# Kernel optimization log

Measured on AMD Instinct MI355X. Metric: run time of the kernel, lower is better.

Reference implementation:

```python
import jax, jax.numpy as jnp
import numpy as np
import math

N = 20000      # nodes
E = 320000     # edges
D = 256        # in_dim == out_dim (residual requires equality)
H = 8          # heads
K = D // H     # k_dim = 32
T = 3          # node types
R = 5          # edge (relation) types
C = 16         # output classes
SQRT_K = math.sqrt(K)


def setup_inputs() -> dict:
    key = jax.random.key(0)
    ks = jax.random.split(key, 18)
    x = jax.random.normal(ks[0], (N, D), jnp.float32)
    edge_index = jax.random.randint(ks[1], (2, E), 0, N, jnp.int32)
    node_type = jax.random.randint(ks[2], (N,), 0, T, jnp.int32)
    edge_type = jax.random.randint(ks[3], (E,), 0, R, jnp.int32)
    g_lin = math.sqrt(2.0 / (D + D))
    g_rel = math.sqrt(2.0 / (K + K))
    g_out = math.sqrt(2.0 / (D + C))
    Wk = jax.random.normal(ks[4], (T, D, D), jnp.float32) * g_lin
    bk = jnp.zeros((T, D), jnp.float32)
    Wq = jax.random.normal(ks[5], (T, D, D), jnp.float32) * g_lin
    bq = jnp.zeros((T, D), jnp.float32)
    Wv = jax.random.normal(ks[6], (T, D, D), jnp.float32) * g_lin
    bv = jnp.zeros((T, D), jnp.float32)
    Wa = jax.random.normal(ks[7], (T, D, D), jnp.float32) * g_lin
    ba = jnp.zeros((T, D), jnp.float32)
    rel_prior = jnp.ones((R, H), jnp.float32)
    rel_att = jax.random.normal(ks[8], (R, H, K, K), jnp.float32) * g_rel
    rel_msg = jax.random.normal(ks[9], (R, H, K, K), jnp.float32) * g_rel
    W_out = jax.random.normal(ks[10], (D, C), jnp.float32) * g_out
    b_out = jnp.zeros((C,), jnp.float32)
    return {"x": x, "edge_index": edge_index, "node_type": node_type,
            "edge_type": edge_type, "Wk": Wk, "bk": bk, "Wq": Wq, "bq": bq,
            "Wv": Wv, "bv": bv, "Wa": Wa, "ba": ba, "rel_prior": rel_prior,
            "rel_att": rel_att, "rel_msg": rel_msg, "W_out": W_out, "b_out": b_out}


def _typed_linear(h, W, b, node_type):
    # per-node-type Linear: small fixed loop over T types, masked select
    out = jnp.zeros((h.shape[0], W.shape[2]), h.dtype)
    for t in range(T):
        m = (node_type == t)[:, None]
        out = out + jnp.where(m, h @ W[t] + b[t], 0.0)
    return out


def _hgt_forward(x, edge_index, node_type, edge_type, Wk, bk, Wq, bq, Wv, bv,
                 Wa, ba, rel_prior, rel_att, rel_msg, W_out, b_out):
    src, dst = edge_index[0], edge_index[1]
    # typed projections -> [N, H, K]
    Kn = _typed_linear(x, Wk, bk, node_type).reshape(N, H, K)
    Qn = _typed_linear(x, Wq, bq, node_type).reshape(N, H, K)
    Vn = _typed_linear(x, Wv, bv, node_type).reshape(N, H, K)
    Ke, Qe, Ve = Kn[src], Qn[dst], Vn[src]  # [E, H, K] gathers
    # relation-specific bilinear transforms of K and V (fixed loop over R)
    Kt = jnp.zeros_like(Ke)
    Mt = jnp.zeros_like(Ve)
    for r in range(R):
        m = (edge_type == r)[:, None, None]
        Kt = Kt + jnp.where(m, jnp.einsum('ehk,hkl->ehl', Ke, rel_att[r]), 0.0)
        Mt = Mt + jnp.where(m, jnp.einsum('ehk,hkl->ehl', Ve, rel_msg[r]), 0.0)
    # attention logits with relation prior, scaled by sqrt(k_dim)
    logits = (Qe * Kt).sum(-1) * rel_prior[edge_type] / SQRT_K  # [E, H]
    # segment softmax over incoming edges per destination node
    mx = jax.ops.segment_max(logits, dst, num_segments=N)       # [N, H]
    ex = jnp.exp(logits - mx[dst])
    sm = jax.ops.segment_sum(ex, dst, num_segments=N)           # [N, H]
    att = ex / sm[dst]                                          # [E, H]
    # weighted messages, scatter-add aggregation
    msg = (Mt * att[:, :, None]).reshape(E, D)
    aggr = jax.ops.segment_sum(msg, dst, num_segments=N)        # [N, D]
    # update: ELU, typed output linear, residual
    h = jax.nn.elu(aggr)
    h = _typed_linear(h, Wa, ba, node_type) + x
    # final classifier + log_softmax
    return jax.nn.log_softmax(h @ W_out + b_out, axis=1)


def reference(x, edge_index, node_type, edge_type, Wk, bk, Wq, bq, Wv, bv,
              Wa, ba, rel_prior, rel_att, rel_msg, W_out, b_out):
    return _hgt_forward(x, edge_index, node_type, edge_type, Wk, bk, Wq, bq,
                        Wv, bv, Wa, ba, rel_prior, rel_att, rel_msg, W_out, b_out)
```

## Files before the change

### kernel.cpp

```cpp
#include <hip/hip_runtime.h>
#include <hip/hip_bf16.h>
#include <math.h>

#define NN 20000
#define NE 320000
#define DD 256
#define NH 8
#define KK 32
#define NR 5
#define NC 16
#define NB2 391

typedef unsigned short u16;
typedef unsigned int u32;
typedef __attribute__((ext_vector_type(8))) short bf16x8;
typedef __attribute__((ext_vector_type(4))) float f32x4;

__device__ __forceinline__ float bf2f(u16 v){ return __uint_as_float(((u32)v)<<16); }
__device__ __forceinline__ u16 f2bf(float f){
  u32 u = __float_as_uint(f);
  return (u16)((u + 0x7FFFu + ((u>>16)&1u)) >> 16);
}

__global__ void k_pre1(const int* __restrict__ ntype, const int* __restrict__ ei,
                       const int* __restrict__ etype, int* __restrict__ cnt,
                       int* __restrict__ off2, int* __restrict__ perm){
  int b = blockIdx.x;
  if(b < 79){
    int n = b*256 + threadIdx.x;
    int t = (n < NN) ? ntype[n] : -1;
    int lane = threadIdx.x & 63;
    #pragma unroll
    for(int tt=0; tt<3; tt++){
      unsigned long long mask = __ballot(t == tt);
      int leader = __ffsll((long long)mask) - 1;
      if(lane == leader) atomicAdd(&cnt[tt], __popcll(mask));
    }
  } else if(b < 1329){
    int e = (b-79)*256 + threadIdx.x;
    if(e < NE) atomicAdd(&off2[ei[NE + e]*NR + etype[e]], 1);
  } else {
    int i = (b-1329)*256 + threadIdx.x;
    if(i < 20096) perm[i] = -1;
  }
}

__global__ __launch_bounds__(256) void k_pre2(int* __restrict__ off2, int* __restrict__ bsum,
                                              const int* __restrict__ cnt, int* __restrict__ boff){
  if(blockIdx.x == NB2){
    if(threadIdx.x == 0){
      int a = (cnt[0]+31)&~31;
      int bb = (cnt[1]+31)&~31;
      boff[0]=0; boff[1]=a; boff[2]=a+bb;
    }
    return;
  }
  __shared__ int sh[256];
  int t = threadIdx.x;
  int i = blockIdx.x*256 + t;
  int v = (i < NN*NR) ? off2[i] : 0;
  sh[t] = v;
  __syncthreads();
  for(int off=1; off<256; off<<=1){
    int val = (t >= off) ? sh[t-off] : 0;
    __syncthreads();
    sh[t] += val;
    __syncthreads();
  }
  if(i < NN*NR) off2[i] = sh[t] - v;
  if(t == 255) bsum[blockIdx.x] = sh[255];
}
__global__ __launch_bounds__(512) void k_scan2(int* __restrict__ bsum, int* __restrict__ off2){
  __shared__ int sh[512];
  int t = threadIdx.x;
  int v = (t < NB2) ? bsum[t] : 0;
  sh[t] = v;
  __syncthreads();
  for(int off=1; off<512; off<<=1){
    int val = (t >= off) ? sh[t-off] : 0;
    __syncthreads();
    sh[t] += val;
    __syncthreads();
  }
  if(t < NB2) bsum[t] = sh[t] - v;
  if(t == 511) off2[NN*NR] = sh[511];
}
__global__ void k_pre3(int* __restrict__ off2, const int* __restrict__ bsum,
                       const int* __restrict__ ntype, const int* __restrict__ boff,
                       int* __restrict__ bcur, int* __restrict__ perm,
                       int* __restrict__ pos2){
  int b = blockIdx.x;
  if(b < NB2){
    int i = b*256 + threadIdx.x;
    if(i < NN*NR) off2[i] += bsum[b];
  } else {
    int n = (b-NB2)*256 + threadIdx.x;
    int t = (n < NN) ? ntype[n] : -1;
    int lane = threadIdx.x & 63;
    #pragma unroll
    for(int tt=0; tt<3; tt++){
      unsigned long long mask = __ballot(t == tt);
      if(t == tt){
        int rank = __popcll(mask & ((1ull<<lane)-1ull));
        int leader = __ffsll((long long)mask) - 1;
        int base = 0;
        if(lane == leader) base = atomicAdd(&bcur[tt], __popcll(mask));
        base = __shfl(base, leader);
        int p = boff[tt] + base + rank;
        perm[p] = n;
        pos2[n] = p;
      }
    }
  }
}

__global__ __launch_bounds__(256) void k_work1(
    const int* __restrict__ ei, const int* __restrict__ etype,
    int* __restrict__ off2, int* __restrict__ packed,
    const float* __restrict__ x, u16* __restrict__ xb,
    const float* __restrict__ Wk, const float* __restrict__ Wq,
    const float* __restrict__ Wv, const float* __restrict__ Wa,
    u16* __restrict__ Wtk, u16* __restrict__ Wtq,
    u16* __restrict__ Wtv, u16* __restrict__ Wta,
    const float* __restrict__ rmsg, const float* __restrict__ ratt,
    const float* __restrict__ prior, const float* __restrict__ Wo,
    u16* __restrict__ Mtm, u16* __restrict__ Atb, u16* __restrict__ Wot)
{
  __shared__ float tile[32][33];
  int b = blockIdx.x;
  if(b < 1250){
    int e = b*256 + threadIdx.x;
    if(e < NE){
      int pos = atomicAdd(&off2[ei[NE+e]*NR + etype[e]], 1);
      packed[pos] = ei[e];
    }
  } else if(b < 3750){
    int i = (b-1250)*256 + threadIdx.x;
    float4 v0 = ((const float4*)x)[i*2+0];
    float4 v1 = ((const float4*)x)[i*2+1];
    uint4 o;
    o.x = (u32)f2bf(v0.x) | ((u32)f2bf(v0.y)<<16);
    o.y = (u32)f2bf(v0.z) | ((u32)f2bf(v0.w)<<16);
    o.z = (u32)f2bf(v1.x) | ((u32)f2bf(v1.y)<<16);
    o.w = (u32)f2bf(v1.z) | ((u32)f2bf(v1.w)<<16);
    ((uint4*)xb)[i] = o;
  } else if(b < 4518){
    int bp = b - 3750;
    int bx = bp & 7, by = (bp>>3) & 7, z = bp >> 6;
    int tensor = z/3, t = z%3;
    const float* W = (tensor==0) ? Wk : (tensor==1) ? Wq : (tensor==2) ? Wv : Wa;
    u16* O = (tensor==0) ? Wtk : (tensor==1) ? Wtq : (tensor==2) ? Wtv : Wta;
    int i0 = bx*32, j0 = by*32;
    int rr = threadIdx.x>>5, cc = threadIdx.x&31;
    #pragma unroll
    for(int p=0;p<4;p++)
      tile[rr+p*8][cc] = W[t*65536 + (i0+rr+p*8)*256 + j0+cc];
    __syncthreads();
    #pragma unroll
    for(int p=0;p<4;p++)
      O[t*65536 + (j0+rr+p*8)*256 + i0+cc] = f2bf(tile[cc][rr+p*8]);
  } else {
    int bp = b - 4518;
    if(bp < 160){
      int idx = bp*256 + threadIdx.x;
      int l = idx & 31, k = (idx >> 5) & 31, rh = idx >> 10;
      Mtm[(rh*32 + l)*32 + k] = f2bf(rmsg[idx]);
    } else if(bp < 320){
      int idx = (bp-160)*256 + threadIdx.x;
      int rh = idx >> 10;
      float scale = prior[rh] * 0.17677669529663687f;
      Atb[idx] = f2bf(ratt[idx] * scale);
    } else {
      int idx = (bp-320)*256 + threadIdx.x;
      int c = idx & 15, k = idx >> 4;
      Wot[c*DD + k] = f2bf(Wo[k*NC + c]);
    }
  }
}

#define XSP 264
__global__ __launch_bounds__(256) void k_projqa(
    const u16* __restrict__ xb, const int* __restrict__ perm, const int* __restrict__ boff,
    const u16* __restrict__ Wtk, const u16* __restrict__ Wtq, const u16* __restrict__ Wtv,
    const float* __restrict__ bk, const float* __restrict__ bq, const float* __restrict__ bv,
    const u16* __restrict__ Atb,
    u16* __restrict__ KVn, u16* __restrict__ QA)
{
  __shared__ u16 smem[32*XSP];
  __shared__ int gids[32];
  int tid = threadIdx.x;
  int ts = (blockIdx.x >> 1)*32;
  int cb = (blockIdx.x & 1)*128;
  int t = (ts >= boff[2]) ? 2 : (ts >= boff[1]) ? 1 : 0;
  if(tid < 32) gids[tid] = perm[ts + tid];
  __syncthreads();
  #pragma unroll
  for(int it=0; it<4; it++){
    int q = tid + it*256;
    int row = q >> 5, c = q & 31;
    int g = gids[row];
    uint4 v = make_uint4(0,0,0,0);
    if(g >= 0) v = ((const uint4*)(xb + (size_t)g*DD))[c];
    ((uint4*)(smem + row*XSP))[c] = v;
  }
  __syncthreads();
  int lane = tid & 63;
  int w = tid >> 6;
  int quad = lane >> 4;
  int l16 = lane & 15;
  f32x4 accK[2][2], accQ[2][2], accV[2][2];
  #pragma unroll
  for(int mt=0;mt<2;mt++)
    #pragma unroll
    for(int nt=0;nt<2;nt++){
      accK[mt][nt]=(f32x4)(0.f); accQ[mt][nt]=(f32x4)(0.f); accV[mt][nt]=(f32x4)(0.f);
    }
  const u16* wkp = Wtk + (size_t)t*65536;
  const u16* wqp = Wtq + (size_t)t*65536;
  const u16* wvp = Wtv + (size_t)t*65536;
  #pragma unroll
  for(int kk=0; kk<8; kk++){
    int kb = kk*32 + quad*8;
    bf16x8 a0 = *(const bf16x8*)(smem + l16*XSP + kb);
    bf16x8 a1 = *(const bf16x8*)(smem + (16+l16)*XSP + kb);
    #pragma unroll
    for(int nt=0; nt<2; nt++){
      int n = cb + w*32 + nt*16 + l16;
      bf16x8 bK = *(const bf16x8*)(wkp + (size_t)n*DD + kb);
      bf16x8 bQ = *(const bf16x8*)(wqp + (size_t)n*DD + kb);
      bf16x8 bV = *(const bf16x8*)(wvp + (size_t)n*DD + kb);
      accK[0][nt] = __builtin_amdgcn_mfma_f32_16x16x32_bf16(a0, bK, accK[0][nt], 0,0,0);
      accK[1][nt] = __builtin_amdgcn_mfma_f32_16x16x32_bf16(a1, bK, accK[1][nt], 0,0,0);
      accQ[0][nt] = __builtin_amdgcn_mfma_f32_16x16x32_bf16(a0, bQ, accQ[0][nt], 0,0,0);
      accQ[1][nt] = __builtin_amdgcn_mfma_f32_16x16x32_bf16(a1, bQ, accQ[1][nt], 0,0,0);
      accV[0][nt] = __builtin_amdgcn_mfma_f32_16x16x32_bf16(a0, bV, accV[0][nt], 0,0,0);
      accV[1][nt] = __builtin_amdgcn_mfma_f32_16x16x32_bf16(a1, bV, accV[1][nt], 0,0,0);
    }
  }
  __syncthreads();
  #pragma unroll
  for(int nt=0; nt<2; nt++){
    int lc = w*32 + nt*16 + l16;
    int colg = cb + lc;
    int kvo = ((lc >> 2)*8 + (lc & 3));
    float bkv = bk[t*DD+colg], bvv = bv[t*DD+colg];
    #pragma unroll
    for(int mt=0; mt<2; mt++){
      #pragma unroll
      for(int reg=0; reg<4; reg++){
        int row = mt*16 + quad*4 + reg;
        smem[row*XSP + kvo]     = f2bf(accK[mt][nt][reg] + bkv);
        smem[row*XSP + kvo + 4] = f2bf(accV[mt][nt][reg] + bvv);
      }
    }
  }
  __syncthreads();
  #pragma unroll
  for(int it=0; it<4; it++){
    int q = tid + it*256;
    int row = q >> 5, c = q & 31;
    int g = gids[row];
    if(g >= 0)
      *(uint4*)(KVn + (size_t)g*512 + (cb>>2)*8 + c*8) = ((uint4*)(smem + row*XSP))[c];
  }
  __syncthreads();
  #pragma unroll
  for(int nt=0; nt<2; nt++){
    int lc = w*32 + nt*16 + l16;
    float bqv = bq[t*DD + cb + lc];
    #pragma unroll
    for(int mt=0; mt<2; mt++){
      #pragma unroll
      for(int reg=0; reg<4; reg++){
        int row = mt*16 + quad*4 + reg;
        smem[row*XSP + lc] = f2bf(accQ[mt][nt][reg] + bqv);
      }
    }
  }
  __syncthreads();
  int h = (cb >> 5) + w;
  bf16x8 qf0 = *(const bf16x8*)(smem + l16*XSP + w*32 + quad*8);
  bf16x8 qf1 = *(const bf16x8*)(smem + (16+l16)*XSP + w*32 + quad*8);
  for(int r=0; r<NR; r++){
    f32x4 acc[2][2];
    #pragma unroll
    for(int mt=0;mt<2;mt++)
      #pragma unroll
      for(int nt=0;nt<2;nt++) acc[mt][nt]=(f32x4)(0.f);
    const u16* ap = Atb + (size_t)(r*NH + h)*1024;
    bf16x8 b0 = *(const bf16x8*)(ap + l16*32 + quad*8);
    bf16x8 b1 = *(const bf16x8*)(ap + (16+l16)*32 + quad*8);
    acc[0][0] = __builtin_amdgcn_mfma_f32_16x16x32_bf16(qf0, b0, acc[0][0], 0,0,0);
    acc[0][1] = __builtin_amdgcn_mfma_f32_16x16x32_bf16(qf0, b1, acc[0][1], 0,0,0);
    acc[1][0] = __builtin_amdgcn_mfma_f32_16x16x32_bf16(qf1, b0, acc[1][0], 0,0,0);
    acc[1][1] = __builtin_amdgcn_mfma_f32_16x16x32_bf16(qf1, b1, acc[1][1], 0,0,0);
    __syncthreads();
    #pragma unroll
    for(int mt=0; mt<2; mt++)
      #pragma unroll
      for(int nt=0; nt<2; nt++)
        #pragma unroll
        for(int reg=0; reg<4; reg++){
          int row = mt*16 + quad*4 + reg;
          smem[row*XSP + w*32 + nt*16 + l16] = f2bf(acc[mt][nt][reg]);
        }
    __syncthreads();
    #pragma unroll
    for(int it=0; it<2; it++){
      int q = tid + it*256;
      int row = q >> 4, c = q & 15;
      int g = gids[row];
      if(g >= 0)
        *(uint4*)(QA + ((size_t)g*NR + r)*DD + cb + c*8) = ((uint4*)(smem + row*XSP))[c];
    }
  }
}

#define VSP 264
__global__ __launch_bounds__(256) void k_edge(
    const u16* __restrict__ KVn, const u16* __restrict__ QA,
    const int* __restrict__ off2, const int* __restrict__ packed,
    const int* __restrict__ pos2, u16* __restrict__ aggrV)
{
  int lane = threadIdx.x & 63;
  int n = blockIdx.x*4 + (threadIdx.x >> 6);
  if(n >= NN) return;
  int off = lane*4;
  float4 qa[NR];
  {
    const u16* qp = QA + (size_t)n*NR*DD + off;
    #pragma unroll
    for(int r=0;r<NR;r++){
      ushort4 q = *(const ushort4*)(qp + r*DD);
      qa[r] = make_float4(bf2f(q.x),bf2f(q.y),bf2f(q.z),bf2f(q.w));
    }
  }
  int eb[NR+1];
  eb[0] = (n==0) ? 0 : off2[n*NR - 1];
  #pragma unroll
  for(int i=1;i<=NR;i++) eb[i] = off2[n*NR + i - 1];
  float4 acc[NR];
  float s = 0.f;
  int lo8 = lane*8;

  #define EDGE_DOT(kv, q, dd) \
    { float k0=__uint_as_float((kv).x<<16), k1=__uint_as_float((kv).x&0xffff0000u); \
      float k2=__uint_as_float((kv).y<<16), k3=__uint_as_float((kv).y&0xffff0000u); \
      dd = k0*(q).x + k1*(q).y + k2*(q).z + k3*(q).w; }
  #define EDGE_ACC(kv, p, a) \
    { float v0=__uint_as_float((kv).z<<16), v1=__uint_as_float((kv).z&0xffff0000u); \
      float v2=__uint_as_float((kv).w<<16), v3=__uint_as_float((kv).w&0xffff0000u); \
      (a).x += (p)*v0; (a).y += (p)*v1; (a).z += (p)*v2; (a).w += (p)*v3; }
  #define RED3(d) { d += __shfl_xor(d,1); d += __shfl_xor(d,2); d += __shfl_xor(d,4); }

  #pragma unroll
  for(int r=0;r<NR;r++){
    float4 q = qa[r];
    float4 a = make_float4(0.f,0.f,0.f,0.f);
    int e = eb[r], end = eb[r+1];
    for(; e+4 <= end; e += 4){
      int s0 = packed[e], s1 = packed[e+1], s2 = packed[e+2], s3 = packed[e+3];
      uint4 kv0 = *(const uint4*)(KVn + (size_t)s0*512 + lo8);
      uint4 kv1 = *(const uint4*)(KVn + (size_t)s1*512 + lo8);
      uint4 kv2 = *(const uint4*)(KVn + (size_t)s2*512 + lo8);
      uint4 kv3 = *(const uint4*)(KVn + (size_t)s3*512 + lo8);
      float d0,d1,d2,d3;
      EDGE_DOT(kv0,q,d0); EDGE_DOT(kv1,q,d1); EDGE_DOT(kv2,q,d2); EDGE_DOT(kv3,q,d3);
      RED3(d0); RED3(d1); RED3(d2); RED3(d3);
      float p0=__expf(d0), p1=__expf(d1), p2=__expf(d2), p3=__expf(d3);
      s += p0 + p1 + p2 + p3;
      EDGE_ACC(kv0,p0,a); EDGE_ACC(kv1,p1,a); EDGE_ACC(kv2,p2,a); EDGE_ACC(kv3,p3,a);
    }
    if(e+2 <= end){
      int s0 = packed[e], s1 = packed[e+1];
      uint4 kv0 = *(const uint4*)(KVn + (size_t)s0*512 + lo8);
      uint4 kv1 = *(const uint4*)(KVn + (size_t)s1*512 + lo8);
      float d0,d1;
      EDGE_DOT(kv0,q,d0); EDGE_DOT(kv1,q,d1);
      RED3(d0); RED3(d1);
      float p0=__expf(d0), p1=__expf(d1);
      s += p0 + p1;
      EDGE_ACC(kv0,p0,a); EDGE_ACC(kv1,p1,a);
      e += 2;
    }
    if(e < end){
      int s0 = packed[e];
      uint4 kv0 = *(const uint4*)(KVn + (size_t)s0*512 + lo8);
      float d0;
      EDGE_DOT(kv0,q,d0);
      RED3(d0);
      float p0=__expf(d0);
      s += p0;
      EDGE_ACC(kv0,p0,a);
    }
    acc[r] = a;
  }
  #undef EDGE_DOT
  #undef EDGE_ACC
  #undef RED3
  float inv = (s > 0.f) ? (1.f/s) : 0.f;
  int p = pos2[n];
  u16* op = aggrV + (size_t)p*NR*DD + off;
  #pragma unroll
  for(int r=0;r<NR;r++){
    ushort4 o;
    o.x=f2bf(acc[r].x*inv); o.y=f2bf(acc[r].y*inv);
    o.z=f2bf(acc[r].z*inv); o.w=f2bf(acc[r].w*inv);
    *(ushort4*)(op + r*DD) = o;
  }
}

__global__ __launch_bounds__(256) void k_mo(
    const u16* __restrict__ aggrV, const u16* __restrict__ Mtm,
    const float* __restrict__ x,
    const int* __restrict__ perm, const int* __restrict__ boff,
    const u16* __restrict__ Wta, const float* __restrict__ ba,
    const u16* __restrict__ Wot, const float* __restrict__ bo,
    float* __restrict__ out)
{
  __shared__ u16 Vs[32*VSP];
  __shared__ u16 hs[32*VSP];
  __shared__ u16 h2s[32*VSP];
  __shared__ int gids[32];
  int tid = threadIdx.x;
  int ts = blockIdx.x*32;
  int t = (ts >= boff[2]) ? 2 : (ts >= boff[1]) ? 1 : 0;
  if(tid < 32) gids[tid] = perm[ts + tid];
  __syncthreads();
  int lane = tid & 63, w = tid >> 6, quad = lane >> 4, l16 = lane & 15;

  f32x4 macc[2][2][2];
  #pragma unroll
  for(int hh=0;hh<2;hh++)
    #pragma unroll
    for(int mt=0;mt<2;mt++)
      #pragma unroll
      for(int nt=0;nt<2;nt++) macc[hh][mt][nt]=(f32x4)(0.f);
  #pragma unroll
  for(int r=0;r<NR;r++){
    u16* B = (r & 1) ? h2s : Vs;
    #pragma unroll
    for(int it=0; it<4; it++){
      int q = tid + it*256;
      int row = q >> 5, c = q & 31;
      ((uint4*)(B + row*VSP))[c] =
        ((const uint4*)(aggrV + ((size_t)(ts+row)*NR + r)*DD))[c];
    }
    __syncthreads();
    #pragma unroll
    for(int hh=0; hh<2; hh++){
      int h = w*2 + hh;
      bf16x8 a0 = *(const bf16x8*)(B + l16*VSP + h*32 + quad*8);
      bf16x8 a1 = *(const bf16x8*)(B + (16+l16)*VSP + h*32 + quad*8);
      const u16* mp = Mtm + ((size_t)(r*NH + h)*32)*32;
      bf16x8 b0 = *(const bf16x8*)(mp + l16*32 + quad*8);
      bf16x8 b1 = *(const bf16x8*)(mp + (16+l16)*32 + quad*8);
      macc[hh][0][0] = __builtin_amdgcn_mfma_f32_16x16x32_bf16(a0, b0, macc[hh][0][0], 0,0,0);
      macc[hh][0][1] = __builtin_amdgcn_mfma_f32_16x16x32_bf16(a0, b1, macc[hh][0][1], 0,0,0);
      macc[hh][1][0] = __builtin_amdgcn_mfma_f32_16x16x32_bf16(a1, b0, macc[hh][1][0], 0,0,0);
      macc[hh][1][1] = __builtin_amdgcn_mfma_f32_16x16x32_bf16(a1, b1, macc[hh][1][1], 0,0,0);
    }
  }
  #pragma unroll
  for(int hh=0; hh<2; hh++){
    int h = w*2 + hh;
    #pragma unroll
    for(int mt=0; mt<2; mt++){
      #pragma unroll
      for(int nt=0; nt<2; nt++){
        #pragma unroll
        for(int reg=0; reg<4; reg++){
          int row = mt*16 + quad*4 + reg;
          float v = macc[hh][mt][nt][reg];
          v = (v > 0.f) ? v : expm1f(v);
          hs[row*VSP + h*32 + nt*16 + l16] = f2bf(v);
        }
      }
    }
  }
  __syncthreads();

  f32x4 acc[2][4];
  #pragma unroll
  for(int mt=0;mt<2;mt++)
    #pragma unroll
    for(int nt=0;nt<4;nt++) acc[mt][nt]=(f32x4)(0.f);
  const u16* wap = Wta + (size_t)t*65536;
  #pragma unroll
  for(int kk=0; kk<8; kk++){
    int kb = kk*32 + quad*8;
    bf16x8 a0 = *(const bf16x8*)(hs + l16*VSP + kb);
    bf16x8 a1 = *(const bf16x8*)(hs + (16+l16)*VSP + kb);
    #pragma unroll
    for(int nt=0; nt<4; nt++){
      int n = w*64 + nt*16 + l16;
      bf16x8 b = *(const bf16x8*)(wap + (size_t)n*DD + kb);
      acc[0][nt] = __builtin_amdgcn_mfma_f32_16x16x32_bf16(a0, b, acc[0][nt], 0,0,0);
      acc[1][nt] = __builtin_amdgcn_mfma_f32_16x16x32_bf16(a1, b, acc[1][nt], 0,0,0);
    }
  }
  #pragma unroll
  for(int nt=0; nt<4; nt++){
    int colg = w*64 + nt*16 + l16;
    float bav = ba[t*DD + colg];
    #pragma unroll
    for(int mt=0; mt<2; mt++){
      #pragma unroll
      for(int reg=0; reg<4; reg++){
        int row = mt*16 + quad*4 + reg;
        int g = gids[row];
        float xr = (g>=0) ? x[(size_t)g*DD + colg] : 0.f;
        h2s[row*VSP + colg] = f2bf(acc[mt][nt][reg] + bav + xr);
      }
    }
  }
  __syncthreads();
  if(w < 2){
    f32x4 cacc = (f32x4)(0.f);
    #pragma unroll
    for(int kk=0; kk<8; kk++){
      int kb = kk*32 + quad*8;
      bf16x8 a = *(const bf16x8*)(h2s + (w*16 + l16)*VSP + kb);
      bf16x8 b = *(const bf16x8*)(Wot + (size_t)l16*DD + kb);
      cacc = __builtin_amdgcn_mfma_f32_16x16x32_bf16(a, b, cacc, 0,0,0);
    }
    float bov = bo[l16];
    #pragma unroll
    for(int reg=0; reg<4; reg++){
      int row = w*16 + quad*4 + reg;
      int g = gids[row];
      float v = cacc[reg] + bov;
      float m = v;
      m = fmaxf(m, __shfl_xor(m,1)); m = fmaxf(m, __shfl_xor(m,2));
      m = fmaxf(m, __shfl_xor(m,4)); m = fmaxf(m, __shfl_xor(m,8));
      float p = __expf(v - m);
      p += __shfl_xor(p,1); p += __shfl_xor(p,2);
      p += __shfl_xor(p,4); p += __shfl_xor(p,8);
      float lse = m + __logf(p);
      if(g >= 0) out[(size_t)g*NC + l16] = v - lse;
    }
  }
}

extern "C" void kernel_launch(void* const* d_in, const int* in_sizes, int n_in,
                              void* d_out, int out_size, void* d_ws, size_t ws_size,
                              hipStream_t stream)
{
  const float* x     = (const float*)d_in[0];
  const int*   ei    = (const int*)d_in[1];
  const int*   ntype = (const int*)d_in[2];
  const int*   etype = (const int*)d_in[3];
  const float* Wk    = (const float*)d_in[4];
  const float* bk    = (const float*)d_in[5];
  const float* Wq    = (const float*)d_in[6];
  const float* bq    = (const float*)d_in[7];
  const float* Wv    = (const float*)d_in[8];
  const float* bv    = (const float*)d_in[9];
  const float* Wa    = (const float*)d_in[10];
  const float* ba    = (const float*)d_in[11];
  const float* prior = (const float*)d_in[12];
  const float* ratt  = (const float*)d_in[13];
  const float* rmsg  = (const float*)d_in[14];
  const float* Wo    = (const float*)d_in[15];
  const float* bo    = (const float*)d_in[16];
  float* out = (float*)d_out;

  char* ws = (char*)d_ws;
  int* iw      = (int*)ws;
  int* cnt     = iw + 0;
  int* bcur    = iw + 4;
  int* boff    = iw + 8;
  int* off2    = iw + 16;
  int* perm    = iw + 100032;
  int* packed  = iw + 120128;
  int* bsum    = iw + 440128;
  int* pos2    = iw + 440640;

  size_t fb = 1842688;
  u16*   KVn   = (u16*)(ws + fb);   fb += 2ull*NN*512;
  u16*   QA    = (u16*)(ws + fb);   fb += 2ull*NN*NR*DD;
  u16*   aggrV = (u16*)(ws + fb);   fb += 2ull*20096*NR*DD;
  u16*   Wtk   = (u16*)(ws + fb);   fb += 2ull*3*65536;
  u16*   Wtq   = (u16*)(ws + fb);   fb += 2ull*3*65536;
  u16*   Wtv   = (u16*)(ws + fb);   fb += 2ull*3*65536;
  u16*   Wta   = (u16*)(ws + fb);   fb += 2ull*3*65536;
  u16*   Wot   = (u16*)(ws + fb);   fb += 2ull*NC*DD;
  u16*   Mtm   = (u16*)(ws + fb);   fb += 2ull*NR*NH*KK*KK;
  u16*   Atb   = (u16*)(ws + fb);   fb += 2ull*NR*NH*KK*KK;
  u16* xb = aggrV;

  hipMemsetAsync(iw, 0, (size_t)(16 + NN*NR + 1)*sizeof(int), stream);

  k_pre1   <<<1408, 256, 0, stream>>>(ntype, ei, etype, cnt, off2, perm);
  k_pre2   <<<NB2+1, 256, 0, stream>>>(off2, bsum, cnt, boff);
  k_scan2  <<<1, 512, 0, stream>>>(bsum, off2);
  k_pre3   <<<NB2+79, 256, 0, stream>>>(off2, bsum, ntype, boff, bcur, perm, pos2);
  k_work1  <<<4854, 256, 0, stream>>>(ei, etype, off2, packed, x, xb,
                                      Wk, Wq, Wv, Wa, Wtk, Wtq, Wtv, Wta,
                                      rmsg, ratt, prior, Wo, Mtm, Atb, Wot);
  k_projqa <<<1256, 256, 0, stream>>>(xb, perm, boff, Wtk, Wtq, Wtv, bk, bq, bv,
                                      Atb, KVn, QA);
  k_edge   <<<5000, 256, 0, stream>>>(KVn, QA, off2, packed, pos2, aggrV);
  k_mo     <<<628, 256, 0, stream>>>(aggrV, Mtm, x, perm, boff, Wta, ba, Wot, bo, out);
}
```

Baseline: 291.6 us.

## Store node features in type-sorted order and split Q·rel_att into separate kernel

Result: slower. 305.3 us (+4.7%).

```diff
diff --git a/kernel.cpp b/kernel.cpp
--- a/kernel.cpp
+++ b/kernel.cpp
@@ -10,6 +10,7 @@
 #define NR 5
 #define NC 16
 #define NB2 391
+#define NPAD 20096
 
 typedef unsigned short u16;
 typedef unsigned int u32;
@@ -41,7 +42,7 @@
     if(e < NE) atomicAdd(&off2[ei[NE + e]*NR + etype[e]], 1);
   } else {
     int i = (b-1329)*256 + threadIdx.x;
-    if(i < 20096) perm[i] = -1;
+    if(i < NPAD) perm[i] = -1;
   }
 }
 
@@ -117,6 +118,7 @@
 __global__ __launch_bounds__(256) void k_work1(
     const int* __restrict__ ei, const int* __restrict__ etype,
     int* __restrict__ off2, int* __restrict__ packed,
+    const int* __restrict__ pos2,
     const float* __restrict__ x, u16* __restrict__ xb,
     const float* __restrict__ Wk, const float* __restrict__ Wq,
     const float* __restrict__ Wv, const float* __restrict__ Wa,
@@ -132,7 +134,7 @@
     int e = b*256 + threadIdx.x;
     if(e < NE){
       int pos = atomicAdd(&off2[ei[NE+e]*NR + etype[e]], 1);
-      packed[pos] = ei[e];
+      packed[pos] = pos2[ei[e]];
     }
   } else if(b < 3750){
     int i = (b-1250)*256 + threadIdx.x;
@@ -183,8 +185,7 @@
     const u16* __restrict__ xb, const int* __restrict__ perm, const int* __restrict__ boff,
     const u16* __restrict__ Wtk, const u16* __restrict__ Wtq, const u16* __restrict__ Wtv,
     const float* __restrict__ bk, const float* __restrict__ bq, const float* __restrict__ bv,
-    const u16* __restrict__ Atb,
-    u16* __restrict__ KVn, u16* __restrict__ QA)
+    u16* __restrict__ KVn, u16* __restrict__ Qn)
 {
   __shared__ u16 smem[32*XSP];
   __shared__ int gids[32];
@@ -259,9 +260,7 @@
   for(int it=0; it<4; it++){
     int q = tid + it*256;
     int row = q >> 5, c = q & 31;
-    int g = gids[row];
-    if(g >= 0)
-      *(uint4*)(KVn + (size_t)g*512 + (cb>>2)*8 + c*8) = ((uint4*)(smem + row*XSP))[c];
+    *(uint4*)(KVn + (size_t)(ts+row)*512 + (cb>>2)*8 + c*8) = ((uint4*)(smem + row*XSP))[c];
   }
   __syncthreads();
   #pragma unroll
@@ -278,23 +277,55 @@
     }
   }
   __syncthreads();
-  int h = (cb >> 5) + w;
-  bf16x8 qf0 = *(const bf16x8*)(smem + l16*XSP + w*32 + quad*8);
-  bf16x8 qf1 = *(const bf16x8*)(smem + (16+l16)*XSP + w*32 + quad*8);
-  for(int r=0; r<NR; r++){
-    f32x4 acc[2][2];
+  #pragma unroll
+  for(int it=0; it<2; it++){
+    int q = tid + it*256;
+    int row = q >> 4, c = q & 15;
+    *(uint4*)(Qn + (size_t)(ts+row)*DD + cb + c*8) = ((uint4*)(smem + row*XSP))[c];
+  }
+}
+
+#define QSP 264
+__global__ __launch_bounds__(256) void k_qa(
+    const u16* __restrict__ Qn, const u16* __restrict__ Atb, u16* __restrict__ QA)
+{
+  __shared__ u16 qs[32*QSP];
+  int tid = threadIdx.x;
+  int tile = blockIdx.x / NR;
+  int r = blockIdx.x - tile*NR;
+  int ts = tile*32;
+  #pragma unroll
+  for(int it=0; it<4; it++){
+    int q = tid + it*256;
+    int row = q >> 5, c = q & 31;
+    ((uint4*)(qs + row*QSP))[c] = ((const uint4*)(Qn + (size_t)(ts+row)*DD))[c];
+  }
+  __syncthreads();
+  int lane = tid & 63, w = tid >> 6, quad = lane >> 4, l16 = lane & 15;
+  f32x4 acc[2][2][2];
+  #pragma unroll
+  for(int hh=0;hh<2;hh++)
     #pragma unroll
     for(int mt=0;mt<2;mt++)
       #pragma unroll
-      for(int nt=0;nt<2;nt++) acc[mt][nt]=(f32x4)(0.f);
+      for(int nt=0;nt<2;nt++) acc[hh][mt][nt]=(f32x4)(0.f);
+  #pragma unroll
+  for(int hh=0; hh<2; hh++){
+    int h = w*2 + hh;
+    bf16x8 a0 = *(const bf16x8*)(qs + l16*QSP + h*32 + quad*8);
+    bf16x8 a1 = *(const bf16x8*)(qs + (16+l16)*QSP + h*32 + quad*8);
     const u16* ap = Atb + (size_t)(r*NH + h)*1024;
     bf16x8 b0 = *(const bf16x8*)(ap + l16*32 + quad*8);
     bf16x8 b1 = *(const bf16x8*)(ap + (16+l16)*32 + quad*8);
-    acc[0][0] = __builtin_amdgcn_mfma_f32_16x16x32_bf16(qf0, b0, acc[0][0], 0,0,0);
-    acc[0][1] = __builtin_amdgcn_mfma_f32_16x16x32_bf16(qf0, b1, acc[0][1], 0,0,0);
-    acc[1][0] = __builtin_amdgcn_mfma_f32_16x16x32_bf16(qf1, b0, acc[1][0], 0,0,0);
-    acc[1][1] = __builtin_amdgcn_mfma_f32_16x16x32_bf16(qf1, b1, acc[1][1], 0,0,0);
-    __syncthreads();
+    acc[hh][0][0] = __builtin_amdgcn_mfma_f32_16x16x32_bf16(a0, b0, acc[hh][0][0], 0,0,0);
+    acc[hh][0][1] = __builtin_amdgcn_mfma_f32_16x16x32_bf16(a0, b1, acc[hh][0][1], 0,0,0);
+    acc[hh][1][0] = __builtin_amdgcn_mfma_f32_16x16x32_bf16(a1, b0, acc[hh][1][0], 0,0,0);
+    acc[hh][1][1] = __builtin_amdgcn_mfma_f32_16x16x32_bf16(a1, b1, acc[hh][1][1], 0,0,0);
+  }
+  __syncthreads();
+  #pragma unroll
+  for(int hh=0; hh<2; hh++){
+    int h = w*2 + hh;
     #pragma unroll
     for(int mt=0; mt<2; mt++)
       #pragma unroll
@@ -302,17 +333,15 @@
         #pragma unroll
         for(int reg=0; reg<4; reg++){
           int row = mt*16 + quad*4 + reg;
-          smem[row*XSP + w*32 + nt*16 + l16] = f2bf(acc[mt][nt][reg]);
+          qs[row*QSP + h*32 + nt*16 + l16] = f2bf(acc[hh][mt][nt][reg]);
         }
-    __syncthreads();
-    #pragma unroll
-    for(int it=0; it<2; it++){
-      int q = tid + it*256;
-      int row = q >> 4, c = q & 15;
-      int g = gids[row];
-      if(g >= 0)
-        *(uint4*)(QA + ((size_t)g*NR + r)*DD + cb + c*8) = ((uint4*)(smem + row*XSP))[c];
-    }
+  }
+  __syncthreads();
+  #pragma unroll
+  for(int it=0; it<4; it++){
+    int q = tid + it*256;
+    int row = q >> 5, c = q & 31;
+    *(uint4*)(QA + ((size_t)(ts+row)*NR + r)*DD + c*8) = ((uint4*)(qs + row*QSP))[c];
   }
 }
 
@@ -320,15 +349,17 @@
 __global__ __launch_bounds__(256) void k_edge(
     const u16* __restrict__ KVn, const u16* __restrict__ QA,
     const int* __restrict__ off2, const int* __restrict__ packed,
-    const int* __restrict__ pos2, u16* __restrict__ aggrV)
+    const int* __restrict__ perm, u16* __restrict__ aggrV)
 {
   int lane = threadIdx.x & 63;
-  int n = blockIdx.x*4 + (threadIdx.x >> 6);
-  if(n >= NN) return;
+  int p = blockIdx.x*4 + (threadIdx.x >> 6);
+  if(p >= NPAD) return;
+  int n = perm[p];
+  if(n < 0) return;
   int off = lane*4;
   float4 qa[NR];
   {
-    const u16* qp = QA + (size_t)n*NR*DD + off;
+    const u16* qp = QA + (size_t)p*NR*DD + off;
     #pragma unroll
     for(int r=0;r<NR;r++){
       ushort4 q = *(const ushort4*)(qp + r*DD);
@@ -399,7 +430,6 @@
   #undef EDGE_ACC
   #undef RED3
   float inv = (s > 0.f) ? (1.f/s) : 0.f;
-  int p = pos2[n];
   u16* op = aggrV + (size_t)p*NR*DD + off;
   #pragma unroll
   for(int r=0;r<NR;r++){
@@ -577,9 +607,10 @@
   int* pos2    = iw + 440640;
 
   size_t fb = 1842688;
-  u16*   KVn   = (u16*)(ws + fb);   fb += 2ull*NN*512;
-  u16*   QA    = (u16*)(ws + fb);   fb += 2ull*NN*NR*DD;
-  u16*   aggrV = (u16*)(ws + fb);   fb += 2ull*20096*NR*DD;
+  u16*   KVn   = (u16*)(ws + fb);   fb += 2ull*NPAD*512;
+  u16*   Qn    = (u16*)(ws + fb);   fb += 2ull*NPAD*DD;
+  u16*   QA    = (u16*)(ws + fb);   fb += 2ull*NPAD*NR*DD;
+  u16*   aggrV = (u16*)(ws + fb);   fb += 2ull*NPAD*NR*DD;
   u16*   Wtk   = (u16*)(ws + fb);   fb += 2ull*3*65536;
   u16*   Wtq   = (u16*)(ws + fb);   fb += 2ull*3*65536;
   u16*   Wtv   = (u16*)(ws + fb);   fb += 2ull*3*65536;
@@ -595,11 +626,12 @@
   k_pre2   <<<NB2+1, 256, 0, stream>>>(off2, bsum, cnt, boff);
   k_scan2  <<<1, 512, 0, stream>>>(bsum, off2);
   k_pre3   <<<NB2+79, 256, 0, stream>>>(off2, bsum, ntype, boff, bcur, perm, pos2);
-  k_work1  <<<4854, 256, 0, stream>>>(ei, etype, off2, packed, x, xb,
+  k_work1  <<<4854, 256, 0, stream>>>(ei, etype, off2, packed, pos2, x, xb,
                                       Wk, Wq, Wv, Wa, Wtk, Wtq, Wtv, Wta,
                                       rmsg, ratt, prior, Wo, Mtm, Atb, Wot);
   k_projqa <<<1256, 256, 0, stream>>>(xb, perm, boff, Wtk, Wtq, Wtv, bk, bq, bv,
-                                      Atb, KVn, QA);
-  k_edge   <<<5000, 256, 0, stream>>>(KVn, QA, off2, packed, pos2, aggrV);
+                                      KVn, Qn);
+  k_qa     <<<628*NR, 256, 0, stream>>>(Qn, Atb, QA);
+  k_edge   <<<5024, 256, 0, stream>>>(KVn, QA, off2, packed, perm, aggrV);
   k_mo     <<<628, 256, 0, stream>>>(aggrV, Mtm, x, perm, boff, Wta, ba, Wot, bo, out);
 }
```
